# Performance work log

Hardware: AMD Instinct MI355X
Metric: run time of the kernel (lower is better)

The kernel has to match this reference:

```python
import jax, jax.numpy as jnp
import numpy as np

T, B, D_IN, D_H = 2048, 64, 256, 256


def setup_inputs() -> dict:
    key = jax.random.key(0)
    ks = jax.random.split(key, 6)
    s = 1.0 / np.sqrt(D_H)  # nn.RNNCell default init scale (uniform); use scaled normal for test data
    return {
        "x": jax.random.normal(ks[0], (T, B, D_IN), dtype=jnp.float32),
        "hx": jax.random.normal(ks[1], (B, D_H), dtype=jnp.float32),
        "W_ih": jax.random.normal(ks[2], (D_H, D_IN), dtype=jnp.float32) * s,
        "W_hh": jax.random.normal(ks[3], (D_H, D_H), dtype=jnp.float32) * s,
        "b_ih": jax.random.normal(ks[4], (D_H,), dtype=jnp.float32) * s,
        "b_hh": jax.random.normal(ks[5], (D_H,), dtype=jnp.float32) * s,
    }


def reference(x, hx, W_ih, W_hh, b_ih, b_hh):
    # RNNCell: h' = tanh(x_t @ W_ih^T + b_ih + h @ W_hh^T + b_hh)
    # Precompute the input projection for all timesteps in one big GEMM.
    xproj = jnp.einsum("tbi,hi->tbh", x, W_ih) + b_ih + b_hh  # [T, B, H]

    def step(h, xp_t):
        h_new = jnp.tanh(xp_t + h @ W_hh.T)
        return h_new, h_new

    h_last, outputs = jax.lax.scan(step, hx, xproj)
    return outputs, h_last  # outputs: [T, B, H] (stacked per-step hidden states)
```

## Files before the change

kernel.cpp:

```cpp
#include <hip/hip_runtime.h>
#include <hip/hip_bf16.h>

#define T_STEPS 2048
#define BATCH   64
#define DIN     256
#define DH      256

#define P1_BM 128
#define P1_BN 128
#define P1_KC 32
#define P1_PAD 4

__global__ __launch_bounds__(256) void xproj_kernel(
    const float* __restrict__ x, const float* __restrict__ W,
    const float* __restrict__ b_ih, const float* __restrict__ b_hh,
    float* __restrict__ out) {
  __shared__ float As[P1_KC][P1_BM + P1_PAD];
  __shared__ float Wt[P1_KC][P1_BN + P1_PAD];
  const int tid = threadIdx.x;
  const int m0 = blockIdx.x * P1_BM;
  const int j0 = blockIdx.y * P1_BN;
  const int r0 = (tid >> 4) * 8;
  const int c0 = (tid & 15) * 8;
  float acc[8][8] = {};

  for (int kc = 0; kc < DIN; kc += P1_KC) {
    __syncthreads();
#pragma unroll
    for (int s = 0; s < 4; ++s) {
      int idx = s * 256 + tid;
      int row = idx >> 3;
      int c4  = (idx & 7) << 2;
      float4 v = *reinterpret_cast<const float4*>(
          &x[(size_t)(m0 + row) * DIN + kc + c4]);
      As[c4 + 0][row] = v.x; As[c4 + 1][row] = v.y;
      As[c4 + 2][row] = v.z; As[c4 + 3][row] = v.w;
    }
#pragma unroll
    for (int s = 0; s < 4; ++s) {
      int idx = s * 256 + tid;
      int row = idx >> 3;
      int c4  = (idx & 7) << 2;
      float4 v = *reinterpret_cast<const float4*>(
          &W[(size_t)(j0 + row) * DIN + kc + c4]);
      Wt[c4 + 0][row] = v.x; Wt[c4 + 1][row] = v.y;
      Wt[c4 + 2][row] = v.z; Wt[c4 + 3][row] = v.w;
    }
    __syncthreads();
#pragma unroll
    for (int k = 0; k < P1_KC; ++k) {
      float4 a0 = *reinterpret_cast<const float4*>(&As[k][r0]);
      float4 a1 = *reinterpret_cast<const float4*>(&As[k][r0 + 4]);
      float4 w0 = *reinterpret_cast<const float4*>(&Wt[k][c0]);
      float4 w1 = *reinterpret_cast<const float4*>(&Wt[k][c0 + 4]);
      float a[8] = {a0.x, a0.y, a0.z, a0.w, a1.x, a1.y, a1.z, a1.w};
      float wv[8] = {w0.x, w0.y, w0.z, w0.w, w1.x, w1.y, w1.z, w1.w};
#pragma unroll
      for (int i = 0; i < 8; ++i)
#pragma unroll
        for (int jj = 0; jj < 8; ++jj)
          acc[i][jj] = fmaf(a[i], wv[jj], acc[i][jj]);
    }
  }

  float bias[8];
#pragma unroll
  for (int jj = 0; jj < 8; ++jj) bias[jj] = b_ih[j0 + c0 + jj] + b_hh[j0 + c0 + jj];
#pragma unroll
  for (int i = 0; i < 8; ++i) {
    size_t m = (size_t)(m0 + r0 + i);
#pragma unroll
    for (int j4 = 0; j4 < 2; ++j4) {
      float4 v;
      v.x = acc[i][j4 * 4 + 0] + bias[j4 * 4 + 0];
      v.y = acc[i][j4 * 4 + 1] + bias[j4 * 4 + 1];
      v.z = acc[i][j4 * 4 + 2] + bias[j4 * 4 + 2];
      v.w = acc[i][j4 * 4 + 3] + bias[j4 * 4 + 3];
      *reinterpret_cast<float4*>(&out[m * DH + j0 + c0 + j4 * 4]) = v;
    }
  }
}

__global__ __launch_bounds__(512) void rnn_scan_kernel(
    const float* __restrict__ hx, const float* __restrict__ W_hh,
    float* __restrict__ outbuf,
    float* __restrict__ hlast) {
  const int b    = blockIdx.x;
  const int tid  = threadIdx.x;
  const int wave = tid >> 6;
  const int lane = tid & 63;
  const int kg   = lane & 15;
  const int jg   = wave * 4 + (lane >> 4);
  const int jred = jg * 8 + ((lane & 1) << 2) + (lane & 2) + ((lane >> 2) & 1);

  float4 w[8][4];
#pragma unroll
  for (int r = 0; r < 8; ++r)
#pragma unroll
    for (int c = 0; c < 4; ++c)
      w[r][c] = *reinterpret_cast<const float4*>(
          &W_hh[(size_t)(jg * 8 + r) * DH + kg * 16 + c * 4]);

  __shared__ float hbuf[2][4][16][4];
  if (tid < DH) hbuf[0][(tid >> 2) & 3][tid >> 4][tid & 3] = hx[(size_t)b * DH + tid];

  const size_t stride_t = (size_t)BATCH * DH;
  const size_t base     = (size_t)b * DH;

  float xp_next = outbuf[base + jred];
  __syncthreads();

#pragma unroll 1
  for (int t = 0; t < T_STEPS; ++t) {
    const float xp = xp_next;
    if (t + 1 < T_STEPS)
      xp_next = outbuf[(size_t)(t + 1) * stride_t + base + jred];

    const int cur = t & 1;
    float4 hc[4];
#pragma unroll
    for (int c = 0; c < 4; ++c)
      hc[c] = *reinterpret_cast<const float4*>(&hbuf[cur][c][kg][0]);

    float p[8];
#pragma unroll
    for (int r = 0; r < 8; ++r) {
      float a = 0.f;
#pragma unroll
      for (int c = 0; c < 4; ++c) {
        a = fmaf(w[r][c].x, hc[c].x, a);
        a = fmaf(w[r][c].y, hc[c].y, a);
        a = fmaf(w[r][c].z, hc[c].z, a);
        a = fmaf(w[r][c].w, hc[c].w, a);
      }
      p[r] = a;
    }

    const bool b0 = lane & 1, b1 = lane & 2, b2 = lane & 4;
    float q[4];
#pragma unroll
    for (int i = 0; i < 4; ++i) {
      float sent = b0 ? p[i] : p[4 + i];
      float recv = __shfl_xor(sent, 1);
      q[i] = (b0 ? p[4 + i] : p[i]) + recv;
    }
    float u[2];
#pragma unroll
    for (int i = 0; i < 2; ++i) {
      float sent = b1 ? q[i] : q[2 + i];
      float recv = __shfl_xor(sent, 2);
      u[i] = (b1 ? q[2 + i] : q[i]) + recv;
    }
    float sent = b2 ? u[0] : u[1];
    float v = (b2 ? u[1] : u[0]) + __shfl_xor(sent, 4);
    v += __shfl_xor(v, 8);

    const float s = v + xp;
    const float e = __expf(2.0f * s);
    const float h = 1.0f - 2.0f * __builtin_amdgcn_rcpf(e + 1.0f);

    if (!(lane & 8)) {
      hbuf[cur ^ 1][(jred >> 2) & 3][jred >> 4][jred & 3] = h;
      outbuf[(size_t)t * stride_t + base + jred] = h;
    }
    __syncthreads();
  }

  if (tid < DH)
    hlast[base + tid] = hbuf[0][(tid >> 2) & 3][tid >> 4][tid & 3];
}

extern "C" void kernel_launch(void* const* d_in, const int* in_sizes, int n_in,
                              void* d_out, int out_size, void* d_ws, size_t ws_size,
                              hipStream_t stream) {
  const float* x    = (const float*)d_in[0];
  const float* hx   = (const float*)d_in[1];
  const float* W_ih = (const float*)d_in[2];
  const float* W_hh = (const float*)d_in[3];
  const float* b_ih = (const float*)d_in[4];
  const float* b_hh = (const float*)d_in[5];
  float* out   = (float*)d_out;
  float* hlast = out + (size_t)T_STEPS * BATCH * DH;

  dim3 g1((T_STEPS * BATCH) / P1_BM, DH / P1_BN);
  xproj_kernel<<<g1, 256, 0, stream>>>(x, W_ih, b_ih, b_hh, out);

  rnn_scan_kernel<<<BATCH, 512, 0, stream>>>(hx, W_hh, out, hlast);
}
```

Before: 1.786 ms.

## Batch scan xproj loads and h stores over 8-step blocks with lightweight barrier

The recurrent scan loop is restructured into fully unrolled 8-step super-blocks with two ping-pong register buffers. Input-projection values are prefetched a whole block ahead and hidden outputs are stored a block late. A custom barrier waits only on LDS counters (lgkmcnt) rather than all memory, so global loads and stores can stay in flight across per-step barriers instead of sitting on the serial critical path. This adds register pressure (launch bounds set to one block per SM) and relies on the barrier being sufficient for LDS-only synchronisation.

```diff
diff --git a/kernel.cpp b/kernel.cpp
--- a/kernel.cpp
+++ b/kernel.cpp
@@ -5,6 +5,13 @@
 #define BATCH   64
 #define DIN     256
 #define DH      256
+#define ST      (BATCH * DH)
+
+__device__ __forceinline__ void wg_barrier() {
+  asm volatile("s_waitcnt lgkmcnt(0)" ::: "memory");
+  __builtin_amdgcn_s_barrier();
+  asm volatile("" ::: "memory");
+}
 
 #define P1_BM 128
 #define P1_BN 128
@@ -81,7 +88,75 @@
   }
 }
 
-__global__ __launch_bounds__(512) void rnn_scan_kernel(
+
+#define RNN_STEP(i, XP, H)                                                     \
+  {                                                                            \
+    const float4 hc0 = *reinterpret_cast<const float4*>(&hbuf[(i) & 1][0][kg][0]); \
+    const float4 hc1 = *reinterpret_cast<const float4*>(&hbuf[(i) & 1][1][kg][0]); \
+    const float4 hc2 = *reinterpret_cast<const float4*>(&hbuf[(i) & 1][2][kg][0]); \
+    const float4 hc3 = *reinterpret_cast<const float4*>(&hbuf[(i) & 1][3][kg][0]); \
+    float p[8];                                                                \
+    _Pragma("unroll")                                                          \
+    for (int r = 0; r < 8; ++r) {                                              \
+      float a = 0.f;                                                           \
+      a = fmaf(w[r][0].x, hc0.x, a); a = fmaf(w[r][0].y, hc0.y, a);            \
+      a = fmaf(w[r][0].z, hc0.z, a); a = fmaf(w[r][0].w, hc0.w, a);            \
+      a = fmaf(w[r][1].x, hc1.x, a); a = fmaf(w[r][1].y, hc1.y, a);            \
+      a = fmaf(w[r][1].z, hc1.z, a); a = fmaf(w[r][1].w, hc1.w, a);            \
+      a = fmaf(w[r][2].x, hc2.x, a); a = fmaf(w[r][2].y, hc2.y, a);            \
+      a = fmaf(w[r][2].z, hc2.z, a); a = fmaf(w[r][2].w, hc2.w, a);            \
+      a = fmaf(w[r][3].x, hc3.x, a); a = fmaf(w[r][3].y, hc3.y, a);            \
+      a = fmaf(w[r][3].z, hc3.z, a); a = fmaf(w[r][3].w, hc3.w, a);            \
+      p[r] = a;                                                                \
+    }                                                                          \
+    float q[4];                                                                \
+    _Pragma("unroll")                                                          \
+    for (int ii = 0; ii < 4; ++ii) {                                           \
+      float sent = b0 ? p[ii] : p[4 + ii];                                     \
+      float recv = __shfl_xor(sent, 1);                                        \
+      q[ii] = (b0 ? p[4 + ii] : p[ii]) + recv;                                 \
+    }                                                                          \
+    float u[2];                                                                \
+    _Pragma("unroll")                                                          \
+    for (int ii = 0; ii < 2; ++ii) {                                           \
+      float sent = b1 ? u##_dummy_q(q, ii) : q[2 + ii];                        \
+      float recv = __shfl_xor(sent, 2);                                        \
+      u[ii] = (b1 ? q[2 + ii] : q[ii]) + recv;                                 \
+    }                                                                          \
+    float sent = b2 ? u[0] : u[1];                                             \
+    float v = (b2 ? u[1] : u[0]) + __shfl_xor(sent, 4);                        \
+    v += __shfl_xor(v, 8);                                                     \
+    const float s = v + XP[i];                                                 \
+    const float e = __expf(2.0f * s);                                          \
+    const float h = 1.0f - 2.0f * __builtin_amdgcn_rcpf(e + 1.0f);             \
+    H[i] = h;                                                                  \
+    if (writer) hbuf[((i) & 1) ^ 1][wslot][jred >> 4][jred & 3] = h;           \
+    wg_barrier();                                                              \
+  }
+
+#define u_dummy_q(q, ii) q[ii]
+
+#define RNN_SUPER(XP, H)                                                       \
+  RNN_STEP(0, XP, H) RNN_STEP(1, XP, H) RNN_STEP(2, XP, H) RNN_STEP(3, XP, H)  \
+  RNN_STEP(4, XP, H) RNN_STEP(5, XP, H) RNN_STEP(6, XP, H) RNN_STEP(7, XP, H)
+
+#define RNN_STORE8(K, H)                                                       \
+  {                                                                            \
+    if (writer) {                                                              \
+      _Pragma("unroll")                                                        \
+      for (int i = 0; i < 8; ++i)                                              \
+        outbuf[(size_t)((K) * 8 + i) * ST + base + jred] = H[i];               \
+    }                                                                          \
+  }
+
+#define RNN_LOAD8(K, XP)                                                       \
+  {                                                                            \
+    _Pragma("unroll")                                                          \
+    for (int i = 0; i < 8; ++i)                                                \
+      XP[i] = outbuf[(size_t)((K) * 8 + i) * ST + base + jred];                \
+  }
+
+__global__ __launch_bounds__(512, 1) void rnn_scan_kernel(
     const float* __restrict__ hx, const float* __restrict__ W_hh,
     float* __restrict__ outbuf,
     float* __restrict__ hlast) {
@@ -92,6 +167,9 @@
   const int kg   = lane & 15;
   const int jg   = wave * 4 + (lane >> 4);
   const int jred = jg * 8 + ((lane & 1) << 2) + (lane & 2) + ((lane >> 2) & 1);
+  const bool b0 = lane & 1, b1 = lane & 2, b2 = lane & 4;
+  const bool writer = !(lane & 8);
+  const int  wslot  = (jred >> 2) & 3;
 
   float4 w[8][4];
 #pragma unroll
@@ -104,70 +182,26 @@
   __shared__ float hbuf[2][4][16][4];
   if (tid < DH) hbuf[0][(tid >> 2) & 3][tid >> 4][tid & 3] = hx[(size_t)b * DH + tid];
 
-  const size_t stride_t = (size_t)BATCH * DH;
-  const size_t base     = (size_t)b * DH;
-
-  float xp_next = outbuf[base + jred];
+  const size_t base = (size_t)b * DH;
+
+  float xpa[8], xpb[8], ha[8], hb[8];
+  RNN_LOAD8(0, xpa)
+  RNN_LOAD8(1, xpb)
   __syncthreads();
 
 #pragma unroll 1
-  for (int t = 0; t < T_STEPS; ++t) {
-    const float xp = xp_next;
-    if (t + 1 < T_STEPS)
-      xp_next = outbuf[(size_t)(t + 1) * stride_t + base + jred];
-
-    const int cur = t & 1;
-    float4 hc[4];
-#pragma unroll
-    for (int c = 0; c < 4; ++c)
-      hc[c] = *reinterpret_cast<const float4*>(&hbuf[cur][c][kg][0]);
-
-    float p[8];
-#pragma unroll
-    for (int r = 0; r < 8; ++r) {
-      float a = 0.f;
-#pragma unroll
-      for (int c = 0; c < 4; ++c) {
-        a = fmaf(w[r][c].x, hc[c].x, a);
-        a = fmaf(w[r][c].y, hc[c].y, a);
-        a = fmaf(w[r][c].z, hc[c].z, a);
-        a = fmaf(w[r][c].w, hc[c].w, a);
-      }
-      p[r] = a;
-    }
-
-    const bool b0 = lane & 1, b1 = lane & 2, b2 = lane & 4;
-    float q[4];
-#pragma unroll
-    for (int i = 0; i < 4; ++i) {
-      float sent = b0 ? p[i] : p[4 + i];
-      float recv = __shfl_xor(sent, 1);
-      q[i] = (b0 ? p[4 + i] : p[i]) + recv;
-    }
-    float u[2];
-#pragma unroll
-    for (int i = 0; i < 2; ++i) {
-      float sent = b1 ? q[i] : q[2 + i];
-      float recv = __shfl_xor(sent, 2);
-      u[i] = (b1 ? q[2 + i] : q[i]) + recv;
-    }
-    float sent = b2 ? u[0] : u[1];
-    float v = (b2 ? u[1] : u[0]) + __shfl_xor(sent, 4);
-    v += __shfl_xor(v, 8);
-
-    const float s = v + xp;
-    const float e = __expf(2.0f * s);
-    const float h = 1.0f - 2.0f * __builtin_amdgcn_rcpf(e + 1.0f);
-
-    if (!(lane & 8)) {
-      hbuf[cur ^ 1][(jred >> 2) & 3][jred >> 4][jred & 3] = h;
-      outbuf[(size_t)t * stride_t + base + jred] = h;
-    }
-    __syncthreads();
-  }
-
-  if (tid < DH)
-    hlast[base + tid] = hbuf[0][(tid >> 2) & 3][tid >> 4][tid & 3];
+  for (int kk = 0; kk < 128; ++kk) {
+    if (kk > 0) { RNN_STORE8(2 * kk - 1, hb) }
+    RNN_SUPER(xpa, ha)
+    if (kk < 127) { RNN_LOAD8(2 * kk + 2, xpa) }
+    RNN_STORE8(2 * kk, ha)
+    RNN_SUPER(xpb, hb)
+    if (kk < 127) { RNN_LOAD8(2 * kk + 3, xpb) }
+  }
+  RNN_STORE8(255, hb)
+  if (writer) hlast[base + jred] = hb[7];
+
+  (void)wave;
 }
 
 extern "C" void kernel_launch(void* const* d_in, const int* in_sizes, int n_in,
```

After: 1.825 ms. 2.2% more time.
